# Optimization experiments

Hardware: AMD Instinct MI355X
Metric: run time of the kernel (lower is better)

Reference implementation:

```python
import jax, jax.numpy as jnp
import numpy as np

# BEV geometric-kernel-attention shapes
SPATIAL = np.array([[92, 160], [46, 80], [23, 40], [12, 20]], dtype=np.int64)
LEVEL_START = np.concatenate([[0], np.cumsum(SPATIAL[:, 0] * SPATIAL[:, 1])[:-1]]).astype(np.int64)
NUM_VALUE = int((SPATIAL[:, 0] * SPATIAL[:, 1]).sum())  # 19560
B, NQ, H, L, P, D = 1, 20000, 8, 4, 8, 32


def setup_inputs() -> dict:
    key = jax.random.key(0)
    k1, k2, k3 = jax.random.split(key, 3)
    value = jax.random.normal(k1, (B, NUM_VALUE, H, D), dtype=jnp.float32)
    sampling_locations = jax.random.uniform(k2, (B, NQ, H, L, P, 2), dtype=jnp.float32)
    attention_weights = jax.random.uniform(k3, (B, NQ, H, L, P), dtype=jnp.float32)
    attention_weights = attention_weights / attention_weights.sum(axis=(-2, -1), keepdims=True)
    return {
        "value": value,
        "spatial_shapes": jnp.asarray(SPATIAL),
        "level_start_index": jnp.asarray(LEVEL_START),
        "sampling_locations": sampling_locations,
        "attention_weights": attention_weights,
    }


def _gka(value, spatial_shapes, level_start_index, sampling_locations, attention_weights):
    # value: [B, Nv, H, D]; locations: [B, Nq, H, L, P, 2] normalized to [0,1]
    b, nv, h, d = value.shape
    nq, l, p = sampling_locations.shape[1], sampling_locations.shape[3], sampling_locations.shape[4]
    Hs = spatial_shapes[:, 0]  # [L]
    Ws = spatial_shapes[:, 1]
    x = sampling_locations[..., 0]  # [B,Nq,H,L,P]
    y = sampling_locations[..., 1]
    # GKT: nearest/integer (geometric) sampling: floor(loc * size)
    col = jnp.floor(x * Ws[None, None, None, :, None].astype(x.dtype)).astype(jnp.int32)
    row = jnp.floor(y * Hs[None, None, None, :, None].astype(y.dtype)).astype(jnp.int32)
    valid = (col >= 0) & (col < Ws[None, None, None, :, None]) & \
            (row >= 0) & (row < Hs[None, None, None, :, None])
    flat = level_start_index[None, None, None, :, None] + row * Ws[None, None, None, :, None] + col
    flat = jnp.clip(flat, 0, nv - 1)  # [B,Nq,H,L,P] int
    # gather per (batch, head): value_t [B,H,Nv,D]
    v = jnp.transpose(value, (0, 2, 1, 3))
    idx = jnp.transpose(flat, (0, 2, 1, 3, 4)).reshape(b, h, nq * l * p)
    sampled = jnp.take_along_axis(v, idx[..., None], axis=2)  # [B,H,Nq*L*P,D]
    sampled = sampled.reshape(b, h, nq, l, p, d)
    w = jnp.transpose(attention_weights, (0, 2, 1, 3, 4)) * \
        jnp.transpose(valid, (0, 2, 1, 3, 4)).astype(attention_weights.dtype)  # [B,H,Nq,L,P]
    out = jnp.einsum('bhqlp,bhqlpd->bhqd', w, sampled)  # weighted reduce over levels/points
    return jnp.transpose(out, (0, 2, 1, 3)).reshape(b, nq, h * d)


def reference(value, spatial_shapes, level_start_index, sampling_locations, attention_weights):
    out = _gka(value, spatial_shapes, level_start_index, sampling_locations, attention_weights)
    # module returns (output1, output2) from Func and FuncLoad variants — identical math
    return (out, out)
```

## Files before the change

### kernel.cpp

```cpp
#include <hip/hip_runtime.h>


#define GKA_NQ       20000
#define GKA_H        8
#define GKA_NV       19560
#define GKA_OUT_HALF 5120000

__global__ __launch_bounds__(256) void gka_kernel(
    const float* __restrict__ value,
    const float* __restrict__ sloc,
    const float* __restrict__ awgt,
    float* __restrict__ out)
{
    __shared__ uint2 fw[32][34];

    const int tid  = threadIdx.x;
    const int lane = tid & 63;
    const int wave = tid >> 6;
    const int h      = blockIdx.x & 7;
    const int qchunk = blockIdx.x >> 3;
    const int qq   = lane >> 3;
    const int sub  = lane & 7;
    const int qloc = wave * 8 + qq;
    const int q    = qchunk * 32 + qloc;

    const int lvl = sub >> 1;
    const int Wi  = (lvl == 0) ? 160 : (lvl == 1) ? 80 : (lvl == 2) ? 40 : 20;
    const int Hi  = (lvl == 0) ? 92  : (lvl == 1) ? 46 : (lvl == 2) ? 23 : 12;
    const int ls  = (lvl == 0) ? 0   : (lvl == 1) ? 14720 : (lvl == 2) ? 18400 : 19320;
    const float Wf = (float)Wi;
    const float Hf = (float)Hi;

    const int qh = q * GKA_H + h;
    const float4* lp = (const float4*)(sloc + (size_t)qh * 64 + sub * 8);
    const float4 xy0 = lp[0];
    const float4 xy1 = lp[1];
    const float4 w4  = *(const float4*)(awgt + (size_t)qh * 32 + sub * 4);

    {
        const float xs[4] = {xy0.x, xy0.z, xy1.x, xy1.z};
        const float ys[4] = {xy0.y, xy0.w, xy1.y, xy1.w};
        const float ws[4] = {w4.x, w4.y, w4.z, w4.w};
        #pragma unroll
        for (int k = 0; k < 4; ++k) {
            const int col = (int)floorf(xs[k] * Wf);
            const int row = (int)floorf(ys[k] * Hf);
            const bool valid = (col >= 0) & (col < Wi) & (row >= 0) & (row < Hi);
            int f = ls + row * Wi + col;
            f = min(max(f, 0), GKA_NV - 1);
            const float wv = valid ? ws[k] : 0.0f;
            fw[qloc][4 * sub + k] = make_uint2((unsigned)f, __float_as_uint(wv));
        }
    }

    __syncthreads();

    float4 acc = make_float4(0.f, 0.f, 0.f, 0.f);
    const float* vbase = value + h * 32 + sub * 4;
    const uint4* row = (const uint4*)(&fw[qloc][0]);
    #pragma unroll
    for (int jj = 0; jj < 16; ++jj) {
        const uint4 pw = row[jj];
        {
            const float4 v = *(const float4*)(vbase + (size_t)pw.x * 256);
            const float w = __uint_as_float(pw.y);
            acc.x = fmaf(w, v.x, acc.x);
            acc.y = fmaf(w, v.y, acc.y);
            acc.z = fmaf(w, v.z, acc.z);
            acc.w = fmaf(w, v.w, acc.w);
        }
        {
            const float4 v = *(const float4*)(vbase + (size_t)pw.z * 256);
            const float w = __uint_as_float(pw.w);
            acc.x = fmaf(w, v.x, acc.x);
            acc.y = fmaf(w, v.y, acc.y);
            acc.z = fmaf(w, v.z, acc.z);
            acc.w = fmaf(w, v.w, acc.w);
        }
    }

    float* o = out + (size_t)q * 256 + h * 32 + sub * 4;
    *(float4*)o = acc;
    *(float4*)(o + GKA_OUT_HALF) = acc;
}

extern "C" void kernel_launch(void* const* d_in, const int* in_sizes, int n_in,
                              void* d_out, int out_size, void* d_ws, size_t ws_size,
                              hipStream_t stream) {
    const float* value = (const float*)d_in[0];
    const float* sloc  = (const float*)d_in[3];
    const float* awgt  = (const float*)d_in[4];
    float* out = (float*)d_out;

    dim3 grid((GKA_NQ / 32) * GKA_H);
    gka_kernel<<<grid, 256, 0, stream>>>(value, sloc, awgt, out);
}
```

Before: 44.86 us.

## Convert value tensor to bf16 in workspace and gather bf16 rows

Adds a pre-pass kernel that converts the fp32 value tensor to bf16 in the workspace. The main kernel then gathers 8-byte bf16 vectors instead of 16-byte fp32 vectors, with the loads batched eight at a time to expose more memory-level parallelism. This halves the bytes per random gather, but adds a conversion pass over about 20 MB of input plus an extra launch, and introduces bf16 rounding error in the sampled values. The fp32 path remains as a fallback when the workspace is too small.

```diff
diff --git a/kernel.cpp b/kernel.cpp
--- a/kernel.cpp
+++ b/kernel.cpp
@@ -4,9 +4,116 @@
 #define GKA_NQ       20000
 #define GKA_H        8
 #define GKA_NV       19560
+#define GKA_NVAL     5007360
 #define GKA_OUT_HALF 5120000
 
-__global__ __launch_bounds__(256) void gka_kernel(
+static __device__ __forceinline__ unsigned short f2bf(float x) {
+    unsigned u = __float_as_uint(x);
+    unsigned r = 0x7FFFu + ((u >> 16) & 1u);
+    return (unsigned short)((u + r) >> 16);
+}
+static __device__ __forceinline__ float bf2f(unsigned short b) {
+    return __uint_as_float(((unsigned)b) << 16);
+}
+
+__global__ __launch_bounds__(256) void gka_conv(
+    const float* __restrict__ v, ushort* __restrict__ o)
+{
+    const int n4 = GKA_NVAL / 4;
+    for (int i = blockIdx.x * 256 + threadIdx.x; i < n4; i += gridDim.x * 256) {
+        const float4 f = ((const float4*)v)[i];
+        ushort4 b;
+        b.x = f2bf(f.x); b.y = f2bf(f.y); b.z = f2bf(f.z); b.w = f2bf(f.w);
+        ((ushort4*)o)[i] = b;
+    }
+}
+
+__global__ __launch_bounds__(256) void gka_kernel_bf16(
+    const ushort* __restrict__ value,
+    const float* __restrict__ sloc,
+    const float* __restrict__ awgt,
+    float* __restrict__ out)
+{
+    __shared__ uint2 fw[32][34];
+
+    const int tid  = threadIdx.x;
+    const int lane = tid & 63;
+    const int wave = tid >> 6;
+    const int h      = blockIdx.x & 7;
+    const int qchunk = blockIdx.x >> 3;
+    const int qq   = lane >> 3;
+    const int sub  = lane & 7;
+    const int qloc = wave * 8 + qq;
+    const int q    = qchunk * 32 + qloc;
+
+    const int lvl = sub >> 1;
+    const int Wi  = (lvl == 0) ? 160 : (lvl == 1) ? 80 : (lvl == 2) ? 40 : 20;
+    const int Hi  = (lvl == 0) ? 92  : (lvl == 1) ? 46 : (lvl == 2) ? 23 : 12;
+    const int ls  = (lvl == 0) ? 0   : (lvl == 1) ? 14720 : (lvl == 2) ? 18400 : 19320;
+    const float Wf = (float)Wi;
+    const float Hf = (float)Hi;
+
+    const int qh = q * GKA_H + h;
+    const float4* lp = (const float4*)(sloc + (size_t)qh * 64 + sub * 8);
+    const float4 xy0 = lp[0];
+    const float4 xy1 = lp[1];
+    const float4 w4  = *(const float4*)(awgt + (size_t)qh * 32 + sub * 4);
+
+    {
+        const float xs[4] = {xy0.x, xy0.z, xy1.x, xy1.z};
+        const float ys[4] = {xy0.y, xy0.w, xy1.y, xy1.w};
+        const float ws[4] = {w4.x, w4.y, w4.z, w4.w};
+        #pragma unroll
+        for (int k = 0; k < 4; ++k) {
+            const int col = (int)floorf(xs[k] * Wf);
+            const int row = (int)floorf(ys[k] * Hf);
+            const bool valid = (col >= 0) & (col < Wi) & (row >= 0) & (row < Hi);
+            int f = ls + row * Wi + col;
+            f = min(max(f, 0), GKA_NV - 1);
+            const float wv = valid ? ws[k] : 0.0f;
+            fw[qloc][4 * sub + k] = make_uint2((unsigned)f, __float_as_uint(wv));
+        }
+    }
+
+    __syncthreads();
+
+    float4 acc = make_float4(0.f, 0.f, 0.f, 0.f);
+    const ushort* vbase = value + h * 32 + sub * 4;
+    const uint4* row = (const uint4*)(&fw[qloc][0]);
+
+    #pragma unroll
+    for (int b = 0; b < 4; ++b) {
+        uint4 p[4];
+        #pragma unroll
+        for (int t = 0; t < 4; ++t) p[t] = row[b * 4 + t];
+
+        ushort4 v[8];
+        #pragma unroll
+        for (int t = 0; t < 4; ++t) {
+            v[2 * t]     = *(const ushort4*)(vbase + (size_t)p[t].x * 256);
+            v[2 * t + 1] = *(const ushort4*)(vbase + (size_t)p[t].z * 256);
+        }
+        #pragma unroll
+        for (int t = 0; t < 4; ++t) {
+            const float w0 = __uint_as_float(p[t].y);
+            const float w1 = __uint_as_float(p[t].w);
+            acc.x = fmaf(w0, bf2f(v[2 * t].x), acc.x);
+            acc.y = fmaf(w0, bf2f(v[2 * t].y), acc.y);
+            acc.z = fmaf(w0, bf2f(v[2 * t].z), acc.z);
+            acc.w = fmaf(w0, bf2f(v[2 * t].w), acc.w);
+            acc.x = fmaf(w1, bf2f(v[2 * t + 1].x), acc.x);
+            acc.y = fmaf(w1, bf2f(v[2 * t + 1].y), acc.y);
+            acc.z = fmaf(w1, bf2f(v[2 * t + 1].z), acc.z);
+            acc.w = fmaf(w1, bf2f(v[2 * t + 1].w), acc.w);
+        }
+    }
+
+    float* o = out + (size_t)q * 256 + h * 32 + sub * 4;
+    *(float4*)o = acc;
+    *(float4*)(o + GKA_OUT_HALF) = acc;
+}
+
+__global__ __launch_bounds__(256) void gka_kernel_f32(
     const float* __restrict__ value,
     const float* __restrict__ sloc,
     const float* __restrict__ awgt,
@@ -93,5 +200,12 @@
     float* out = (float*)d_out;
 
     dim3 grid((GKA_NQ / 32) * GKA_H);
-    gka_kernel<<<grid, 256, 0, stream>>>(value, sloc, awgt, out);
-}
+
+    if (ws_size >= (size_t)GKA_NVAL * sizeof(ushort)) {
+        ushort* vbf = (ushort*)d_ws;
+        gka_conv<<<1024, 256, 0, stream>>>(value, vbf);
+        gka_kernel_bf16<<<grid, 256, 0, stream>>>(vbf, sloc, awgt, out);
+    } else {
+        gka_kernel_f32<<<grid, 256, 0, stream>>>(value, sloc, awgt, out);
+    }
+}
```

Result: slower. 48.54 us (+8.2%).
